# Performance work log

Measured on AMD Instinct MI355X. Metric: run time of the kernel, lower is better.

The kernel has to match this reference:

```python
import jax, jax.numpy as jnp
import numpy as np

BINS = 30
MOMENTUM = 0.75
LOSS_WEIGHT = 1.0


def setup_inputs() -> dict:
    key = jax.random.key(0)
    k1, k2 = jax.random.split(key)
    N, C = 8192, 2048
    preds = jax.random.normal(k1, (N, C), dtype=jnp.float32)
    targets = jax.random.randint(k2, (N, C), 0, 2).astype(jnp.int32)  # binary multi-hot
    acc_sum = jnp.zeros((BINS, C), dtype=jnp.float32)  # EMA histogram state
    return {"preds": preds, "targets": targets, "acc_sum": acc_sum}


def reference(preds, targets, acc_sum):
    N, C = preds.shape
    t = targets.astype(preds.dtype)

    # gradient norm g = |sigmoid(p) - t|, detached (weights carry no grad)
    g = jnp.abs(jax.nn.sigmoid(jax.lax.stop_gradient(preds)) - t)

    # bin index: edges[i] = i/BINS, so bin = floor(g*BINS), g=1.0 -> last bin (edge[-1]+=1e-6)
    bin_idx = jnp.clip(jnp.floor(g * BINS).astype(jnp.int32), 0, BINS - 1)  # [N, C]

    # per-label histogram: counts[b, c] = #examples with bin b in column c
    cols = jnp.broadcast_to(jnp.arange(C, dtype=jnp.int32)[None, :], (N, C))
    counts = jnp.zeros((BINS, C), dtype=preds.dtype).at[bin_idx, cols].add(1.0)

    # n[c] = number of non-empty bins for label c
    n = jnp.sum(counts >= 1.0, axis=0).astype(preds.dtype)  # [C]

    # EMA update of the histogram (momentum > 0 branch)
    acc_new = MOMENTUM * acc_sum + (1.0 - MOMENTUM) * counts  # [BINS, C]

    tot = jnp.asarray(float(max(N, 1.0)), preds.dtype)
    weights = tot / acc_new[bin_idx, cols]               # gather per-element density
    weights = weights / jnp.maximum(n, 1.0)[None, :]      # normalize by #valid bins
    weights = jax.lax.stop_gradient(weights)

    # BCE with logits, elementwise: softplus-style stable form
    bce = jnp.logaddexp(0.0, preds) - preds * t
    loss = jnp.mean(weights * bce)
    return loss * LOSS_WEIGHT
```

## Files before the change

### kernel.cpp

```cpp
#include <hip/hip_runtime.h>

#define BINS  30
#define NROWS 8192
#define NCOLS 2048
#define COLS_PER_BLK 256
#define ROWS_PER_BLK 256
#define YSLICES 32

#define FIXED_SCALE 16777216.0f
#define CNT_SHIFT   50
#define SUM_MASK    ((1ull << CNT_SHIFT) - 1)

#define WS_PART  0
#define WS_RED   (YSLICES * BINS * NCOLS * 8)
#define WS_BPART (WS_RED + BINS * NCOLS * 8)

__global__ __launch_bounds__(1024, 4) void k_main(
    const float* __restrict__ preds, const int* __restrict__ targets,
    unsigned long long* __restrict__ part)
{
    __shared__ unsigned long long h[BINS * COLS_PER_BLK];
    const int tid = threadIdx.x;
    for (int i = tid; i < BINS * COLS_PER_BLK; i += 1024) h[i] = 0ull;
    __syncthreads();

    const int wave = tid >> 6;
    const int lane = tid & 63;
    const int colBase = blockIdx.x * COLS_PER_BLK;
    const int col0 = colBase + 4 * lane;
    const int r0   = blockIdx.y * ROWS_PER_BLK + wave * 16;

    const float4* P = (const float4*)(preds   + (size_t)r0 * NCOLS + col0);
    const int4*   T = (const int4*)  (targets + (size_t)r0 * NCOLS + col0);
    const int RV = NCOLS / 4;

    float4 pc0 = P[0], pc1 = P[RV], pc2 = P[2 * RV], pc3 = P[3 * RV];
    int4   tc0 = T[0], tc1 = T[RV], tc2 = T[2 * RV], tc3 = T[3 * RV];

    #pragma unroll
    for (int q = 0; q < 4; ++q) {
        float4 pn0, pn1, pn2, pn3;
        int4   tn0, tn1, tn2, tn3;
        if (q < 3) {
            P += 4 * RV; T += 4 * RV;
            pn0 = P[0]; pn1 = P[RV]; pn2 = P[2 * RV]; pn3 = P[3 * RV];
            tn0 = T[0]; tn1 = T[RV]; tn2 = T[2 * RV]; tn3 = T[3 * RV];
        }
        __builtin_amdgcn_sched_barrier(0);

        const float4 pb[4] = {pc0, pc1, pc2, pc3};
        const int4   tb[4] = {tc0, tc1, tc2, tc3};
        #pragma unroll
        for (int r = 0; r < 4; ++r) {
            const float pv[4] = {pb[r].x, pb[r].y, pb[r].z, pb[r].w};
            const int   tv[4] = {tb[r].x, tb[r].y, tb[r].z, tb[r].w};
            #pragma unroll
            for (int j = 0; j < 4; ++j) {
                float p  = pv[j];
                float pp = tv[j] ? -p : p;
                float e  = __expf(-fabsf(pp));
                float d  = 1.0f + e;
                float r1 = __builtin_amdgcn_rcpf(d);
                float g  = (pp >= 0.0f) ? r1 : e * r1;
                int   b  = (int)(g * 30.0f);
                b = b > (BINS - 1) ? (BINS - 1) : b;
                float bce = fmaxf(pp, 0.0f) + __logf(d);
                unsigned long long pk = (1ull << CNT_SHIFT)
                    | (unsigned long long)(bce * FIXED_SCALE + 0.5f);
                atomicAdd(&h[b * COLS_PER_BLK + (j << 6) + lane], pk);
            }
        }
        pc0 = pn0; pc1 = pn1; pc2 = pn2; pc3 = pn3;
        tc0 = tn0; tc1 = tn1; tc2 = tn2; tc3 = tn3;
    }
    __syncthreads();

    const size_t outBase = (size_t)blockIdx.y * BINS * NCOLS + colBase;
    for (int i = tid; i < BINS * COLS_PER_BLK; i += 1024) {
        const int b = i >> 8;
        const int r = i & 255;
        const int l = r >> 2;
        const int j = r & 3;
        part[outBase + (size_t)b * NCOLS + r] = h[b * COLS_PER_BLK + (j << 6) + l];
    }
}

__global__ __launch_bounds__(256) void k_reduce(
    const unsigned long long* __restrict__ part, unsigned long long* __restrict__ red)
{
    const int id = blockIdx.x * 256 + threadIdx.x;
    const size_t cell = (size_t)id * 2;
    unsigned long long a = 0ull, b = 0ull;
    #pragma unroll 8
    for (int y = 0; y < YSLICES; ++y) {
        const ulonglong2 v = *(const ulonglong2*)(part + (size_t)y * BINS * NCOLS + cell);
        a += v.x; b += v.y;
    }
    ulonglong2* o = (ulonglong2*)(red + cell);
    *o = make_ulonglong2(a, b);
}

__global__ __launch_bounds__(256) void k_colsum(
    const unsigned long long* __restrict__ red,
    const float* __restrict__ acc_sum, float* __restrict__ blockPart)
{
    __shared__ float wave_sums[4];
    const int tid = threadIdx.x;
    const int c   = blockIdx.x * 256 + tid;

    float colsum = 0.0f;
    int n = 0;
    #pragma unroll
    for (int b = 0; b < BINS; ++b) {
        const size_t gidx = (size_t)b * NCOLS + c;
        const unsigned long long v = red[gidx];
        if (v) {
            n += 1;
            float cnt = (float)(unsigned)(v >> CNT_SHIFT);
            float s   = (float)(v & SUM_MASK) * (1.0f / FIXED_SCALE);
            float acc_new = 0.75f * acc_sum[gidx] + 0.25f * cnt;
            colsum += s / acc_new;
        }
    }
    colsum /= (float)((n > 1 ? n : 1) * NCOLS);

    #pragma unroll
    for (int off = 32; off > 0; off >>= 1)
        colsum += __shfl_down(colsum, off, 64);
    if ((tid & 63) == 0) wave_sums[tid >> 6] = colsum;
    __syncthreads();
    if (tid == 0)
        blockPart[blockIdx.x] = wave_sums[0] + wave_sums[1] + wave_sums[2] + wave_sums[3];
}

__global__ void k_final(const float* __restrict__ blockPart, float* __restrict__ out)
{
    double s = 0.0;
    #pragma unroll
    for (int i = 0; i < 8; ++i) s += (double)blockPart[i];
    out[0] = (float)s;
}

extern "C" void kernel_launch(void* const* d_in, const int* in_sizes, int n_in,
                              void* d_out, int out_size, void* d_ws, size_t ws_size,
                              hipStream_t stream)
{
    const float* preds   = (const float*)d_in[0];
    const int*   targets = (const int*)d_in[1];
    const float* acc_sum = (const float*)d_in[2];

    unsigned long long* part = (unsigned long long*)((char*)d_ws + WS_PART);
    unsigned long long* red  = (unsigned long long*)((char*)d_ws + WS_RED);
    float* blockPart         = (float*)((char*)d_ws + WS_BPART);

    dim3 gA(NCOLS / COLS_PER_BLK, NROWS / ROWS_PER_BLK);
    k_main<<<gA, 1024, 0, stream>>>(preds, targets, part);

    k_reduce<<<(BINS * NCOLS / 2) / 256, 256, 0, stream>>>(part, red);

    k_colsum<<<NCOLS / 256, 256, 0, stream>>>(red, acc_sum, blockPart);

    k_final<<<1, 1, 0, stream>>>(blockPart, (float*)d_out);
}
```

Before: 181.5 us.

## Pack histogram count and BCE sum into 32-bit LDS atomics over half-height row tiles

Shrinks the packed shared-memory histogram entry from 64 bits to 32 bits: 8 bits of count and 24 bits of fixed-point BCE sum at scale 16384. Row tiles are halved so the per-block count and sum stay within those fields, and the number of row slices doubles to 64. The occupancy hint rises to 8 blocks per SM. The reduce kernel now unpacks each slice and emits float count and sum arrays for the column-sum kernel. This targets the cost of 64-bit LDS atomics and block-level parallelism, at the price of coarser fixed-point BCE accumulation and twice as many partial slices to reduce.

```diff
diff --git a/kernel.cpp b/kernel.cpp
--- a/kernel.cpp
+++ b/kernel.cpp
@@ -4,54 +4,55 @@
 #define NROWS 8192
 #define NCOLS 2048
 #define COLS_PER_BLK 256
-#define ROWS_PER_BLK 256
-#define YSLICES 32
+#define ROWS_PER_BLK 128
+#define YSLICES 64
 
-#define FIXED_SCALE 16777216.0f
-#define CNT_SHIFT   50
-#define SUM_MASK    ((1ull << CNT_SHIFT) - 1)
+#define FIXED_SCALE 16384.0f
+#define CNT_SHIFT   24
+#define SUM_MASK    ((1u << CNT_SHIFT) - 1)
 
 #define WS_PART  0
-#define WS_RED   (YSLICES * BINS * NCOLS * 8)
-#define WS_BPART (WS_RED + BINS * NCOLS * 8)
+#define WS_CNT   (YSLICES * BINS * NCOLS * 4)
+#define WS_BSUM  (WS_CNT + BINS * NCOLS * 4)
+#define WS_BPART (WS_BSUM + BINS * NCOLS * 4)
 
-__global__ __launch_bounds__(1024, 4) void k_main(
+__global__ __launch_bounds__(1024, 8) void k_main(
     const float* __restrict__ preds, const int* __restrict__ targets,
-    unsigned long long* __restrict__ part)
+    unsigned int* __restrict__ part)
 {
-    __shared__ unsigned long long h[BINS * COLS_PER_BLK];
+    __shared__ unsigned int h[BINS * COLS_PER_BLK];
     const int tid = threadIdx.x;
-    for (int i = tid; i < BINS * COLS_PER_BLK; i += 1024) h[i] = 0ull;
+    for (int i = tid; i < BINS * COLS_PER_BLK; i += 1024) h[i] = 0u;
     __syncthreads();
 
     const int wave = tid >> 6;
     const int lane = tid & 63;
     const int colBase = blockIdx.x * COLS_PER_BLK;
     const int col0 = colBase + 4 * lane;
-    const int r0   = blockIdx.y * ROWS_PER_BLK + wave * 16;
+    const int r0   = blockIdx.y * ROWS_PER_BLK + wave * 8;
 
     const float4* P = (const float4*)(preds   + (size_t)r0 * NCOLS + col0);
     const int4*   T = (const int4*)  (targets + (size_t)r0 * NCOLS + col0);
     const int RV = NCOLS / 4;
 
-    float4 pc0 = P[0], pc1 = P[RV], pc2 = P[2 * RV], pc3 = P[3 * RV];
-    int4   tc0 = T[0], tc1 = T[RV], tc2 = T[2 * RV], tc3 = T[3 * RV];
+    float4 pc0 = P[0], pc1 = P[RV];
+    int4   tc0 = T[0], tc1 = T[RV];
 
     #pragma unroll
     for (int q = 0; q < 4; ++q) {
-        float4 pn0, pn1, pn2, pn3;
-        int4   tn0, tn1, tn2, tn3;
+        float4 pn0, pn1;
+        int4   tn0, tn1;
         if (q < 3) {
-            P += 4 * RV; T += 4 * RV;
-            pn0 = P[0]; pn1 = P[RV]; pn2 = P[2 * RV]; pn3 = P[3 * RV];
-            tn0 = T[0]; tn1 = T[RV]; tn2 = T[2 * RV]; tn3 = T[3 * RV];
+            P += 2 * RV; T += 2 * RV;
+            pn0 = P[0]; pn1 = P[RV];
+            tn0 = T[0]; tn1 = T[RV];
         }
         __builtin_amdgcn_sched_barrier(0);
 
-        const float4 pb[4] = {pc0, pc1, pc2, pc3};
-        const int4   tb[4] = {tc0, tc1, tc2, tc3};
+        const float4 pb[2] = {pc0, pc1};
+        const int4   tb[2] = {tc0, tc1};
         #pragma unroll
-        for (int r = 0; r < 4; ++r) {
+        for (int r = 0; r < 2; ++r) {
             const float pv[4] = {pb[r].x, pb[r].y, pb[r].z, pb[r].w};
             const int   tv[4] = {tb[r].x, tb[r].y, tb[r].z, tb[r].w};
             #pragma unroll
@@ -65,13 +66,13 @@
                 int   b  = (int)(g * 30.0f);
                 b = b > (BINS - 1) ? (BINS - 1) : b;
                 float bce = fmaxf(pp, 0.0f) + __logf(d);
-                unsigned long long pk = (1ull << CNT_SHIFT)
-                    | (unsigned long long)(bce * FIXED_SCALE + 0.5f);
+                unsigned int pk = (1u << CNT_SHIFT)
+                    | (unsigned int)(bce * FIXED_SCALE + 0.5f);
                 atomicAdd(&h[b * COLS_PER_BLK + (j << 6) + lane], pk);
             }
         }
-        pc0 = pn0; pc1 = pn1; pc2 = pn2; pc3 = pn3;
-        tc0 = tn0; tc1 = tn1; tc2 = tn2; tc3 = tn3;
+        pc0 = pn0; pc1 = pn1;
+        tc0 = tn0; tc1 = tn1;
     }
     __syncthreads();
 
@@ -86,22 +87,23 @@
 }
 
 __global__ __launch_bounds__(256) void k_reduce(
-    const unsigned long long* __restrict__ part, unsigned long long* __restrict__ red)
+    const unsigned int* __restrict__ part,
+    float* __restrict__ cnt_f, float* __restrict__ bsum_f)
 {
     const int id = blockIdx.x * 256 + threadIdx.x;
-    const size_t cell = (size_t)id * 2;
-    unsigned long long a = 0ull, b = 0ull;
-    #pragma unroll 8
+    unsigned int cnt = 0u, sm = 0u;
+    #pragma unroll 16
     for (int y = 0; y < YSLICES; ++y) {
-        const ulonglong2 v = *(const ulonglong2*)(part + (size_t)y * BINS * NCOLS + cell);
-        a += v.x; b += v.y;
+        const unsigned int v = part[(size_t)y * BINS * NCOLS + id];
+        cnt += v >> CNT_SHIFT;
+        sm  += v & SUM_MASK;
     }
-    ulonglong2* o = (ulonglong2*)(red + cell);
-    *o = make_ulonglong2(a, b);
+    cnt_f[id]  = (float)cnt;
+    bsum_f[id] = (float)sm * (1.0f / FIXED_SCALE);
 }
 
 __global__ __launch_bounds__(256) void k_colsum(
-    const unsigned long long* __restrict__ red,
+    const float* __restrict__ cnt_f, const float* __restrict__ bsum_f,
     const float* __restrict__ acc_sum, float* __restrict__ blockPart)
 {
     __shared__ float wave_sums[4];
@@ -113,13 +115,11 @@
     #pragma unroll
     for (int b = 0; b < BINS; ++b) {
         const size_t gidx = (size_t)b * NCOLS + c;
-        const unsigned long long v = red[gidx];
-        if (v) {
+        const float cnt = cnt_f[gidx];
+        if (cnt >= 1.0f) {
             n += 1;
-            float cnt = (float)(unsigned)(v >> CNT_SHIFT);
-            float s   = (float)(v & SUM_MASK) * (1.0f / FIXED_SCALE);
             float acc_new = 0.75f * acc_sum[gidx] + 0.25f * cnt;
-            colsum += s / acc_new;
+            colsum += bsum_f[gidx] / acc_new;
         }
     }
     colsum /= (float)((n > 1 ? n : 1) * NCOLS);
@@ -149,16 +149,17 @@
     const int*   targets = (const int*)d_in[1];
     const float* acc_sum = (const float*)d_in[2];
 
-    unsigned long long* part = (unsigned long long*)((char*)d_ws + WS_PART);
-    unsigned long long* red  = (unsigned long long*)((char*)d_ws + WS_RED);
-    float* blockPart         = (float*)((char*)d_ws + WS_BPART);
+    unsigned int* part = (unsigned int*)((char*)d_ws + WS_PART);
+    float* cnt_f       = (float*)((char*)d_ws + WS_CNT);
+    float* bsum_f      = (float*)((char*)d_ws + WS_BSUM);
+    float* blockPart   = (float*)((char*)d_ws + WS_BPART);
 
     dim3 gA(NCOLS / COLS_PER_BLK, NROWS / ROWS_PER_BLK);
     k_main<<<gA, 1024, 0, stream>>>(preds, targets, part);
 
-    k_reduce<<<(BINS * NCOLS / 2) / 256, 256, 0, stream>>>(part, red);
+    k_reduce<<<(BINS * NCOLS) / 256, 256, 0, stream>>>(part, cnt_f, bsum_f);
 
-    k_colsum<<<NCOLS / 256, 256, 0, stream>>>(red, acc_sum, blockPart);
+    k_colsum<<<NCOLS / 256, 256, 0, stream>>>(cnt_f, bsum_f, acc_sum, blockPart);
 
     k_final<<<1, 1, 0, stream>>>(blockPart, (float*)d_out);
 }
```

Measured after the change: 179.6 us. No clear change (-1.0%).
